# Kernel tuning notes

Measured on AMD Instinct MI355X. Metric: run time of the kernel, lower is better.

## Reference

```python
import jax, jax.numpy as jnp
import numpy as np

TOP_K = 8
ROUTED_SCALING_FACTOR = 1.0
EPS = 1e-20


def setup_inputs() -> dict:
    key = jax.random.key(0)
    k1, k2, k3 = jax.random.split(key, 3)
    T, D, E = 8192, 4096, 64
    x = jax.random.normal(k1, (T, D), dtype=jnp.float32)
    gate_weight = jax.random.normal(k2, (E, D), dtype=jnp.float32) * (1.0 / np.sqrt(D))
    bias = jax.random.normal(k3, (E,), dtype=jnp.float32) * 0.1
    return {"x": x, "gate_weight": gate_weight, "bias": bias}


def reference(x, gate_weight, bias):
    # logits: [T, E] = x [T, D] @ gate_weight.T [D, E]
    logits = jnp.einsum('td,ed->te', x.astype(jnp.float32), gate_weight)
    scores = jax.nn.sigmoid(logits)
    biased = scores + bias  # broadcast [E]
    # top-k on biased scores, sorted descending
    _, indices = jax.lax.top_k(biased, TOP_K)  # [T, K]
    selected_scores = jnp.take_along_axis(scores, indices, axis=-1)  # [T, K]
    normalized = selected_scores / (jnp.sum(selected_scores, axis=-1, keepdims=True) + EPS)
    weights = normalized * ROUTED_SCALING_FACTOR
    return (indices, weights)
```

## Files before the change

### kernel.cpp

```cpp
#include <hip/hip_runtime.h>
#include <math.h>
#include <stdint.h>

#define T_TOK 8192
#define DDIM  4096
#define NEXP  64
#define TOPK  8
#define MT    128
#define BK    32
#define RS    2048.0f

typedef __attribute__((ext_vector_type(8))) _Float16 half8;
typedef __attribute__((ext_vector_type(4))) float f32x4;
typedef __attribute__((address_space(3))) uint32_t lds_u32;
typedef const __attribute__((address_space(1))) uint32_t glb_u32;

__global__ __launch_bounds__(256) void pack_w(
    const float* __restrict__ gw, _Float16* __restrict__ wpk)
{
    const int g    = blockIdx.x * 256 + threadIdx.x;
    const int lane = g & 63;
    const int n    = (g >> 6) & 3;
    const int kt   = g >> 8;
    const int e    = n * 16 + (lane & 15);
    const int k    = kt * 32 + (lane >> 4) * 8;

    const float* src = gw + (size_t)e * DDIM + k;
    float4 v0 = *reinterpret_cast<const float4*>(src);
    float4 v1 = *reinterpret_cast<const float4*>(src + 4);
    const float v[8] = {v0.x, v0.y, v0.z, v0.w, v1.x, v1.y, v1.z, v1.w};

    half8 h0, h1;
    #pragma unroll
    for (int j = 0; j < 8; j++) {
        _Float16 a = (_Float16)v[j];
        h0[j] = a;
        h1[j] = (_Float16)((v[j] - (float)a) * RS);
    }
    _Float16* dst = wpk + (size_t)kt * 4096 + (size_t)(n * 2) * 512 + lane * 8;
    *reinterpret_cast<half8*>(dst)       = h0;
    *reinterpret_cast<half8*>(dst + 512) = h1;
}

template<int STEPS, int S>
__global__ __launch_bounds__(512) void gemm_part(
    const float* __restrict__ x, const _Float16* __restrict__ wpk,
    float* __restrict__ part)
{
    __shared__ float    A[2][MT * BK];
    __shared__ _Float16 B[2][4096];

    const int tid  = threadIdx.x;
    const int lane = tid & 63;
    const int wv   = tid >> 6;
    const int wm   = wv & 3;
    const int wn   = wv >> 2;
    const int slc  = blockIdx.x % S;
    const int mt   = blockIdx.x / S;
    const int m0   = mt * MT;
    const int kt0  = slc * STEPS;
    const int am   = lane & 15;
    const int ag   = lane >> 4;

    const int s_row0 = tid >> 3;
    const int s_c    = tid & 7;

#define STAGE(buf_, t_) do {                                                   \
        const size_t koff = (size_t)(kt0 + (t_)) * BK;                         \
        int c0 = s_c ^ (s_row0 & 7);                                           \
        __builtin_amdgcn_global_load_lds(                                      \
            (glb_u32*)(x + (size_t)(m0 + s_row0) * DDIM + koff + c0 * 4),      \
            (lds_u32*)(&A[buf_][tid * 4]), 16, 0, 0);                          \
        int r1 = s_row0 + 64;                                                  \
        int c1 = s_c ^ (r1 & 7);                                               \
        __builtin_amdgcn_global_load_lds(                                      \
            (glb_u32*)(x + (size_t)(m0 + r1) * DDIM + koff + c1 * 4),          \
            (lds_u32*)(&A[buf_][2048 + tid * 4]), 16, 0, 0);                   \
        const _Float16* bs = wpk + (size_t)(kt0 + (t_)) * 4096 + tid * 8;      \
        __builtin_amdgcn_global_load_lds(                                      \
            (glb_u32*)bs, (lds_u32*)(&B[buf_][tid * 8]), 16, 0, 0);            \
    } while (0)

    f32x4 aH[2][2], aM[2][2];
    #pragma unroll
    for (int f = 0; f < 2; f++)
        #pragma unroll
        for (int n = 0; n < 2; n++) {
            aH[f][n] = (f32x4){0.f, 0.f, 0.f, 0.f};
            aM[f][n] = (f32x4){0.f, 0.f, 0.f, 0.f};
        }

    STAGE(0, 0);
    __syncthreads();

    #pragma unroll 2
    for (int t = 0; t < STEPS; t++) {
        const int buf = t & 1;
        if (t + 1 < STEPS) STAGE(buf ^ 1, t + 1);

        half8 B0[2], B1[2];
        #pragma unroll
        for (int nf = 0; nf < 2; nf++) {
            const int nb = ((wn * 2 + nf) * 2) * 512 + lane * 8;
            B0[nf] = *reinterpret_cast<const half8*>(&B[buf][nb]);
            B1[nf] = *reinterpret_cast<const half8*>(&B[buf][nb + 512]);
        }
        #pragma unroll
        for (int f = 0; f < 2; f++) {
            const int row = wm * 32 + f * 16 + am;
            const int sw  = am & 7;
            float4 alo = *reinterpret_cast<const float4*>(
                &A[buf][row * BK + ((ag * 2 + 0) ^ sw) * 4]);
            float4 ahi = *reinterpret_cast<const float4*>(
                &A[buf][row * BK + ((ag * 2 + 1) ^ sw) * 4]);
            const float vv[8] = {alo.x, alo.y, alo.z, alo.w,
                                 ahi.x, ahi.y, ahi.z, ahi.w};
            half8 a0, a1;
            #pragma unroll
            for (int j = 0; j < 8; j++) {
                float v = vv[j];
                _Float16 h = (_Float16)v;
                a0[j] = h;
                a1[j] = (_Float16)((v - (float)h) * RS);
            }
            #pragma unroll
            for (int nf = 0; nf < 2; nf++) {
                aH[f][nf] = __builtin_amdgcn_mfma_f32_16x16x32_f16(a0, B0[nf], aH[f][nf], 0, 0, 0);
                aM[f][nf] = __builtin_amdgcn_mfma_f32_16x16x32_f16(a0, B1[nf], aM[f][nf], 0, 0, 0);
                aM[f][nf] = __builtin_amdgcn_mfma_f32_16x16x32_f16(a1, B0[nf], aM[f][nf], 0, 0, 0);
            }
        }
        __syncthreads();
    }
#undef STAGE

    const float i1 = 1.0f / RS;
    float* po = part + (size_t)slc * T_TOK * NEXP + (size_t)m0 * NEXP;
    #pragma unroll
    for (int f = 0; f < 2; f++)
        #pragma unroll
        for (int nf = 0; nf < 2; nf++)
            #pragma unroll
            for (int r = 0; r < 4; r++)
                po[(size_t)(wm * 32 + f * 16 + ag * 4 + r) * NEXP
                   + (wn * 2 + nf) * 16 + am]
                    = aH[f][nf][r] + aM[f][nf][r] * i1;
}

__global__ __launch_bounds__(256) void reduce_topk(
    const float* __restrict__ part, const float* __restrict__ bias,
    float* __restrict__ out, int S)
{
    const int wave = threadIdx.x >> 6;
    const int lane = threadIdx.x & 63;
    const int j    = blockIdx.x;
    const int g    = j & 7;
    const int q    = j >> 3;
    const int token = g * 128 + (q & 31) * 4 + (q >> 5) * 1024 + wave;
    if (token >= T_TOK) return;

    float logit = 0.f;
    for (int s = 0; s < S; s++)
        logit += part[(size_t)s * T_TOK * NEXP + (size_t)token * NEXP + lane];

    float score  = 1.f / (1.f + expf(-logit));
    float biased = score + bias[lane];

    float my_sc = 0.f;
    int   my_idx = 0;
    float ssum  = 0.f;

    #pragma unroll
    for (int jj = 0; jj < TOPK; jj++) {
        float v = biased;
        int   i = lane;
        #pragma unroll
        for (int off = 32; off >= 1; off >>= 1) {
            float ov = __shfl_xor(v, off);
            int   oi = __shfl_xor(i, off);
            if (ov > v || (ov == v && oi < i)) { v = ov; i = oi; }
        }
        float s_sel = __shfl(score, i);
        ssum += s_sel;
        if (lane == jj) { my_idx = i; my_sc = s_sel; }
        if (lane == i) biased = -INFINITY;
    }

    if (lane < TOPK) {
        out[(size_t)token * TOPK + lane] = (float)my_idx;
        out[(size_t)T_TOK * TOPK + (size_t)token * TOPK + lane]
            = my_sc / (ssum + 1e-20f);
    }
}

extern "C" void kernel_launch(void* const* d_in, const int* in_sizes, int n_in,
                              void* d_out, int out_size, void* d_ws, size_t ws_size,
                              hipStream_t stream) {
    (void)in_sizes; (void)n_in; (void)out_size;
    const float* x    = (const float*)d_in[0];
    const float* gw   = (const float*)d_in[1];
    const float* bias = (const float*)d_in[2];
    float* out = (float*)d_out;
    _Float16* wpk = (_Float16*)d_ws;
    float* part = (float*)(wpk + (size_t)DDIM * NEXP * 2);

    const size_t wpk_bytes = (size_t)DDIM * NEXP * 2 * sizeof(_Float16);
    const size_t per_slice = (size_t)T_TOK * NEXP * sizeof(float);
    int S = 1;
    for (int cand : {8, 4, 2}) {
        if (wpk_bytes + (size_t)cand * per_slice <= ws_size) { S = cand; break; }
    }

    pack_w<<<128, 256, 0, stream>>>(gw, wpk);

    dim3 b1(512);
    switch (S) {
        case 8: gemm_part<16, 8><<<dim3(64 * 8), b1, 0, stream>>>(x, wpk, part); break;
        case 4: gemm_part<32, 4><<<dim3(64 * 4), b1, 0, stream>>>(x, wpk, part); break;
        case 2: gemm_part<64, 2><<<dim3(64 * 2), b1, 0, stream>>>(x, wpk, part); break;
        default: gemm_part<128, 1><<<dim3(64), b1, 0, stream>>>(x, wpk, part); break;
    }

    reduce_topk<<<dim3(T_TOK / 4), 256, 0, stream>>>(part, bias, out, S);
}
```

Measured before the change: 47.28 us.

## Fuse weight fp16 split into GEMM, drop pack kernel and B LDS staging

Removes the separate pack_w kernel and the LDS staging of packed fp16 weights. Each wave now loads its fp32 gate_weight slice straight from global memory every K step and splits it into high and residual fp16 parts in registers. This saves a kernel launch and the weight round-trip through the workspace. In exchange it adds redundant per-block global loads and conversion arithmetic in the inner loop, and those loads are synchronous rather than prefetched.

```diff
diff --git a/kernel.cpp b/kernel.cpp
--- a/kernel.cpp
+++ b/kernel.cpp
@@ -15,40 +15,12 @@
 typedef __attribute__((address_space(3))) uint32_t lds_u32;
 typedef const __attribute__((address_space(1))) uint32_t glb_u32;
 
-__global__ __launch_bounds__(256) void pack_w(
-    const float* __restrict__ gw, _Float16* __restrict__ wpk)
-{
-    const int g    = blockIdx.x * 256 + threadIdx.x;
-    const int lane = g & 63;
-    const int n    = (g >> 6) & 3;
-    const int kt   = g >> 8;
-    const int e    = n * 16 + (lane & 15);
-    const int k    = kt * 32 + (lane >> 4) * 8;
-
-    const float* src = gw + (size_t)e * DDIM + k;
-    float4 v0 = *reinterpret_cast<const float4*>(src);
-    float4 v1 = *reinterpret_cast<const float4*>(src + 4);
-    const float v[8] = {v0.x, v0.y, v0.z, v0.w, v1.x, v1.y, v1.z, v1.w};
-
-    half8 h0, h1;
-    #pragma unroll
-    for (int j = 0; j < 8; j++) {
-        _Float16 a = (_Float16)v[j];
-        h0[j] = a;
-        h1[j] = (_Float16)((v[j] - (float)a) * RS);
-    }
-    _Float16* dst = wpk + (size_t)kt * 4096 + (size_t)(n * 2) * 512 + lane * 8;
-    *reinterpret_cast<half8*>(dst)       = h0;
-    *reinterpret_cast<half8*>(dst + 512) = h1;
-}
-
 template<int STEPS, int S>
 __global__ __launch_bounds__(512) void gemm_part(
-    const float* __restrict__ x, const _Float16* __restrict__ wpk,
+    const float* __restrict__ x, const float* __restrict__ gw,
     float* __restrict__ part)
 {
-    __shared__ float    A[2][MT * BK];
-    __shared__ _Float16 B[2][4096];
+    __shared__ float A[2][MT * BK];
 
     const int tid  = threadIdx.x;
     const int lane = tid & 63;
@@ -65,6 +37,9 @@
     const int s_row0 = tid >> 3;
     const int s_c    = tid & 7;
 
+    const float* gB = gw + (size_t)((wn * 2) * 16 + am) * DDIM
+                    + (size_t)kt0 * BK + ag * 8;
+
 #define STAGE(buf_, t_) do {                                                   \
         const size_t koff = (size_t)(kt0 + (t_)) * BK;                         \
         int c0 = s_c ^ (s_row0 & 7);                                           \
@@ -76,9 +51,6 @@
         __builtin_amdgcn_global_load_lds(                                      \
             (glb_u32*)(x + (size_t)(m0 + r1) * DDIM + koff + c1 * 4),          \
             (lds_u32*)(&A[buf_][2048 + tid * 4]), 16, 0, 0);                   \
-        const _Float16* bs = wpk + (size_t)(kt0 + (t_)) * 4096 + tid * 8;      \
-        __builtin_amdgcn_global_load_lds(                                      \
-            (glb_u32*)bs, (lds_u32*)(&B[buf_][tid * 8]), 16, 0, 0);            \
     } while (0)
 
     f32x4 aH[2][2], aM[2][2];
@@ -101,10 +73,19 @@
         half8 B0[2], B1[2];
         #pragma unroll
         for (int nf = 0; nf < 2; nf++) {
-            const int nb = ((wn * 2 + nf) * 2) * 512 + lane * 8;
-            B0[nf] = *reinterpret_cast<const half8*>(&B[buf][nb]);
-            B1[nf] = *reinterpret_cast<const half8*>(&B[buf][nb + 512]);
-        }
+            const float* bp = gB + (size_t)nf * 16 * DDIM + (size_t)t * BK;
+            float4 u0 = *reinterpret_cast<const float4*>(bp);
+            float4 u1 = *reinterpret_cast<const float4*>(bp + 4);
+            const float bv[8] = {u0.x, u0.y, u0.z, u0.w, u1.x, u1.y, u1.z, u1.w};
+            #pragma unroll
+            for (int j = 0; j < 8; j++) {
+                float v = bv[j];
+                _Float16 h = (_Float16)v;
+                B0[nf][j] = h;
+                B1[nf][j] = (_Float16)((v - (float)h) * RS);
+            }
+        }
+
         #pragma unroll
         for (int f = 0; f < 2; f++) {
             const int row = wm * 32 + f * 16 + am;
@@ -200,25 +181,21 @@
     const float* x    = (const float*)d_in[0];
     const float* gw   = (const float*)d_in[1];
     const float* bias = (const float*)d_in[2];
-    float* out = (float*)d_out;
-    _Float16* wpk = (_Float16*)d_ws;
-    float* part = (float*)(wpk + (size_t)DDIM * NEXP * 2);
-
-    const size_t wpk_bytes = (size_t)DDIM * NEXP * 2 * sizeof(_Float16);
+    float* out  = (float*)d_out;
+    float* part = (float*)d_ws;
+
     const size_t per_slice = (size_t)T_TOK * NEXP * sizeof(float);
     int S = 1;
     for (int cand : {8, 4, 2}) {
-        if (wpk_bytes + (size_t)cand * per_slice <= ws_size) { S = cand; break; }
-    }
-
-    pack_w<<<128, 256, 0, stream>>>(gw, wpk);
+        if ((size_t)cand * per_slice <= ws_size) { S = cand; break; }
+    }
 
     dim3 b1(512);
     switch (S) {
-        case 8: gemm_part<16, 8><<<dim3(64 * 8), b1, 0, stream>>>(x, wpk, part); break;
-        case 4: gemm_part<32, 4><<<dim3(64 * 4), b1, 0, stream>>>(x, wpk, part); break;
-        case 2: gemm_part<64, 2><<<dim3(64 * 2), b1, 0, stream>>>(x, wpk, part); break;
-        default: gemm_part<128, 1><<<dim3(64), b1, 0, stream>>>(x, wpk, part); break;
+        case 8: gemm_part<16, 8><<<dim3(64 * 8), b1, 0, stream>>>(x, gw, part); break;
+        case 4: gemm_part<32, 4><<<dim3(64 * 4), b1, 0, stream>>>(x, gw, part); break;
+        case 2: gemm_part<64, 2><<<dim3(64 * 2), b1, 0, stream>>>(x, gw, part); break;
+        default: gemm_part<128, 1><<<dim3(64), b1, 0, stream>>>(x, gw, part); break;
     }
 
     reduce_topk<<<dim3(T_TOK / 4), 256, 0, stream>>>(part, bias, out, S);
```

New measurement: 61.91 us. +30.9%, slower.
